# Performance work log

Hardware: AMD Instinct MI355X
Metric: run time of the kernel (lower is better)

The kernel has to match this reference:

```python
import jax, jax.numpy as jnp
import numpy as np

NEG = -9e15
ALPHA = 0.2  # leaky relu negative slope


def setup_inputs() -> dict:
    key = jax.random.key(0)
    k1, k2, k3, k4 = jax.random.split(key, 4)
    B, N, d = 8, 2048, 128
    h = jax.random.normal(k1, (B, N, d), dtype=jnp.float32)
    adj = jax.random.randint(k2, (B, N, N), 0, 2, dtype=jnp.int32)
    W = jax.random.normal(k3, (d, d), dtype=jnp.float32) * (1.414 / np.sqrt(d))
    a = jax.random.normal(k4, (2 * d, 1), dtype=jnp.float32) * 0.1
    return {"h": h, "adj": adj, "W": W, "a": a}


def reference(h, adj, W, a):
    d = W.shape[1]
    Wh = jnp.matmul(h, W)                       # [B, N, d]  (dropout p=0 -> identity)
    Wh1 = jnp.matmul(Wh, a[:d])                 # [B, N, 1]
    Wh2 = jnp.matmul(Wh, a[d:])                 # [B, N, 1]
    e = jax.nn.leaky_relu(Wh1 + jnp.swapaxes(Wh2, 1, 2), negative_slope=ALPHA)  # [B, N, N]
    scores = jnp.where(adj > 0, e, NEG)
    attention = jax.nn.softmax(scores, axis=-1)  # [B, N, N]
    h_prime = jnp.matmul(attention, Wh)          # [B, N, d]
    out = h + h_prime                            # residual=True, concat=False
    return out, attention
```

## Files before the change

### kernel.cpp

```cpp
#include <hip/hip_runtime.h>
#include <cstdint>
#include <cstddef>

typedef float  v4f __attribute__((ext_vector_type(4)));
typedef short  v8s __attribute__((ext_vector_type(8)));
typedef int    v4i __attribute__((ext_vector_type(4)));
typedef unsigned int v2u __attribute__((ext_vector_type(2)));

#define BB 8
#define NN 2048
#define DD 128
#define TI 16
#define NEGV (-9e15f)

__device__ __forceinline__ unsigned short f2bf(float x) {
  unsigned u = __float_as_uint(x);
  u = u + 0x7FFFu + ((u >> 16) & 1u);
  return (unsigned short)(u >> 16);
}

__global__ __launch_bounds__(256) void gat_k1(
    const float* __restrict__ h, const float* __restrict__ W, const float* __restrict__ a,
    short* __restrict__ whbT, float* __restrict__ wh1g, float* __restrict__ wh2g)
{
  __shared__ __align__(16) unsigned short wT[DD * 136];
  __shared__ __align__(16) unsigned short staging[DD * 72];

  const int tid  = threadIdx.x;
  const int lane = tid & 63;
  const int wid  = tid >> 6;
  const int m16  = lane & 15;
  const int quad = lane >> 4;
  const int b    = blockIdx.y;
  const int i0   = blockIdx.x * 64;

  {
    const v4f* W4 = (const v4f*)W;
    #pragma unroll
    for (int it = 0; it < 16; it++) {
      int idx = it * 256 + tid;
      int k  = idx >> 5;
      int c4 = (idx & 31) * 4;
      v4f wv = W4[idx];
      #pragma unroll
      for (int q = 0; q < 4; q++)
        wT[(c4 + q) * 136 + k] = f2bf(wv[q]);
    }
  }

  const float* hrow = h + (size_t)(b * NN + i0 + wid * 16 + m16) * DD;
  v8s af[4];
  #pragma unroll
  for (int ks = 0; ks < 4; ks++) {
    v4f x0 = *(const v4f*)(hrow + ks * 32 + quad * 8);
    v4f x1 = *(const v4f*)(hrow + ks * 32 + quad * 8 + 4);
    v8s t;
    t[0] = (short)f2bf(x0.x); t[1] = (short)f2bf(x0.y);
    t[2] = (short)f2bf(x0.z); t[3] = (short)f2bf(x0.w);
    t[4] = (short)f2bf(x1.x); t[5] = (short)f2bf(x1.y);
    t[6] = (short)f2bf(x1.z); t[7] = (short)f2bf(x1.w);
    af[ks] = t;
  }
  __syncthreads();

  v4f acc[8];
  #pragma unroll
  for (int t = 0; t < 8; t++) acc[t] = (v4f){0.f, 0.f, 0.f, 0.f};

  #pragma unroll
  for (int ks = 0; ks < 4; ks++) {
    #pragma unroll
    for (int t = 0; t < 8; t++) {
      v8s bf = *(const v8s*)&wT[(t * 16 + m16) * 136 + ks * 32 + quad * 8];
      acc[t] = __builtin_amdgcn_mfma_f32_16x16x32_bf16(af[ks], bf, acc[t], 0, 0, 0);
    }
  }

  {
    float a1v[8], a2v[8];
    #pragma unroll
    for (int t = 0; t < 8; t++) {
      a1v[t] = a[t * 16 + m16];
      a2v[t] = a[DD + t * 16 + m16];
    }
    #pragma unroll
    for (int r = 0; r < 4; r++) {
      float p1 = 0.f, p2 = 0.f;
      #pragma unroll
      for (int t = 0; t < 8; t++) {
        p1 += acc[t][r] * a1v[t];
        p2 += acc[t][r] * a2v[t];
      }
      #pragma unroll
      for (int off = 8; off > 0; off >>= 1) {
        p1 += __shfl_xor(p1, off);
        p2 += __shfl_xor(p2, off);
      }
      if (m16 == 0) {
        int gi = b * NN + i0 + wid * 16 + quad * 4 + r;
        wh1g[gi] = p1;
        wh2g[gi] = p2;
      }
    }
  }

  #pragma unroll
  for (int t = 0; t < 8; t++)
    #pragma unroll
    for (int r = 0; r < 4; r++)
      staging[(t * 16 + m16) * 72 + wid * 16 + quad * 4 + r] = f2bf(acc[t][r]);
  __syncthreads();

  #pragma unroll
  for (int it = 0; it < 4; it++) {
    int idx = it * 256 + tid;
    int c  = idx >> 3;
    int i8 = idx & 7;
    v8s val = *(const v8s*)&staging[c * 72 + i8 * 8];
    *(v8s*)(whbT + (size_t)b * DD * NN + (size_t)c * NN + i0 + i8 * 8) = val;
  }
}

__global__ __launch_bounds__(256) void gat_k2(
    const float* __restrict__ h, const int* __restrict__ adj,
    const short* __restrict__ whbT, const float* __restrict__ wh1g,
    const float* __restrict__ wh2g, float* __restrict__ out,
    float* __restrict__ attout)
{
  __shared__ __align__(16) float wh2s[NN];
  __shared__ float wh1s[TI];
  __shared__ unsigned int maskw[TI * 64];
  __shared__ float m_s[TI];
  __shared__ float rs_s[TI];
  __shared__ __align__(16) unsigned short atile[2][TI * 72];

  const int tid = threadIdx.x;
  const int lane = tid & 63;
  const int wid = tid >> 6;
  const int b = blockIdx.y;
  const int i0 = blockIdx.x * TI;

  {
    const v4f* w2g4 = (const v4f*)(wh2g + (size_t)b * NN);
    ((v4f*)wh2s)[tid] = w2g4[tid];
    ((v4f*)wh2s)[tid + 256] = w2g4[tid + 256];
  }
  if (tid < TI) wh1s[tid] = wh1g[b * NN + i0 + tid];
  __syncthreads();

  for (int ii = wid; ii < TI; ii += 4) {
    const v4i* arow = (const v4i*)(adj + (size_t)(b * NN + i0 + ii) * NN);
    const float wh1v = wh1s[ii];
    float e[32];
    float m = -INFINITY;
    unsigned mbits = 0u;
    #pragma unroll
    for (int u = 0; u < 8; u++) {
      v4i av = __builtin_nontemporal_load(&arow[u * 64 + lane]);
      v4f w2v = ((const v4f*)wh2s)[u * 64 + lane];
      #pragma unroll
      for (int q = 0; q < 4; q++) {
        bool mk = av[q] > 0;
        float x = wh1v + w2v[q];
        float ev = mk ? (x > 0.f ? x : 0.2f * x) : NEGV;
        e[u * 4 + q] = ev;
        m = fmaxf(m, ev);
        mbits |= (mk ? 1u : 0u) << (u * 4 + q);
      }
    }
    maskw[ii * 64 + lane] = mbits;
    #pragma unroll
    for (int off = 32; off > 0; off >>= 1) m = fmaxf(m, __shfl_xor(m, off));
    float s = 0.f;
    #pragma unroll
    for (int k = 0; k < 32; k++) s += __expf(e[k] - m);
    #pragma unroll
    for (int off = 32; off > 0; off >>= 1) s += __shfl_xor(s, off);
    if (lane == 0) { m_s[ii] = m; rs_s[ii] = 1.f / s; }
  }
  __syncthreads();

  float* attrow_base = attout + (size_t)(b * NN + i0) * NN;
  const short* whbT_b = whbT + (size_t)b * DD * NN;
  const int m16 = lane & 15;
  const int quad = lane >> 4;
  const int irow = tid >> 4;
  const int jq = tid & 15;
  const float wh1v = wh1s[irow];
  const float mi_r = m_s[irow];
  const float rsi_r = rs_s[irow];

  v4f acc[2];
  acc[0] = (v4f){0.f, 0.f, 0.f, 0.f};
  acc[1] = (v4f){0.f, 0.f, 0.f, 0.f};

  for (int jc = 0; jc < 32; jc++) {
    const int j0 = jc * 64;
    const int ubit = (jc >> 2) << 2;
    unsigned short* buf = atile[jc & 1];

    {
      unsigned mw = maskw[irow * 64 + ((jc * 16 + jq) & 63)];
      v4f w2v = ((const v4f*)wh2s)[(j0 >> 2) + jq];
      v4f av;
      unsigned short ab[4];
      #pragma unroll
      for (int q = 0; q < 4; q++) {
        float x = wh1v + w2v[q];
        float ev = ((mw >> (ubit + q)) & 1u) ? (x > 0.f ? x : 0.2f * x) : NEGV;
        float at = __expf(ev - mi_r) * rsi_r;
        av[q] = at;
        ab[q] = f2bf(at);
      }
      __builtin_nontemporal_store(av, (v4f*)(attrow_base + (size_t)irow * NN + j0 + jq * 4));
      v2u uv;
      uv[0] = (unsigned)ab[0] | ((unsigned)ab[1] << 16);
      uv[1] = (unsigned)ab[2] | ((unsigned)ab[3] << 16);
      *(v2u*)&buf[irow * 72 + jq * 4] = uv;
    }

    v8s bfr[2][2];
    #pragma unroll
    for (int ks = 0; ks < 2; ks++)
      #pragma unroll
      for (int t = 0; t < 2; t++)
        bfr[ks][t] = *(const v8s*)(whbT_b + (size_t)((wid * 2 + t) * 16 + m16) * NN
                                   + j0 + ks * 32 + quad * 8);

    __syncthreads();

    #pragma unroll
    for (int ks = 0; ks < 2; ks++) {
      v8s af = *(const v8s*)&buf[m16 * 72 + ks * 32 + quad * 8];
      acc[0] = __builtin_amdgcn_mfma_f32_16x16x32_bf16(af, bfr[ks][0], acc[0], 0, 0, 0);
      acc[1] = __builtin_amdgcn_mfma_f32_16x16x32_bf16(af, bfr[ks][1], acc[1], 0, 0, 0);
    }
  }

  #pragma unroll
  for (int t = 0; t < 2; t++) {
    #pragma unroll
    for (int r = 0; r < 4; r++) {
      size_t gidx = ((size_t)(b * NN + i0 + quad * 4 + r)) * DD + (wid * 2 + t) * 16 + m16;
      out[gidx] = h[gidx] + acc[t][r];
    }
  }
}

extern "C" void kernel_launch(void* const* d_in, const int* in_sizes, int n_in,
                              void* d_out, int out_size, void* d_ws, size_t ws_size,
                              hipStream_t stream) {
  const float* h  = (const float*)d_in[0];
  const int* adj  = (const int*)d_in[1];
  const float* W  = (const float*)d_in[2];
  const float* a  = (const float*)d_in[3];

  float* out    = (float*)d_out;
  float* attout = out + (size_t)BB * NN * DD;

  short* whbT = (short*)d_ws;
  float* wh1  = (float*)((char*)d_ws + (size_t)BB * DD * NN * 2);
  float* wh2  = wh1 + BB * NN;

  gat_k1<<<dim3(NN / 64, BB), 256, 0, stream>>>(h, W, a, whbT, wh1, wh2);
  gat_k2<<<dim3(NN / TI, BB), 256, 0, stream>>>(h, adj, whbT, wh1, wh2, out, attout);
}
```

Measured before the change: 285.2 us.

## Split softmax statistics into separate kernel and split-K the attention-value matmul across waves

Moves the adjacency scan, mask packing and row max/sum computation into a new kernel that writes bit masks and statistics to workspace. The main kernel then has each wave cover a quarter of the key dimension for all 128 output columns, building its MFMA A-operand in registers instead of a shared tile. This removes the per-chunk block barrier. Partial sums are reduced through shared memory before the residual add. It adds a kernel launch and workspace traffic, and raises register and LDS use.

```diff
diff --git a/kernel.cpp b/kernel.cpp
--- a/kernel.cpp
+++ b/kernel.cpp
@@ -5,7 +5,6 @@
 typedef float  v4f __attribute__((ext_vector_type(4)));
 typedef short  v8s __attribute__((ext_vector_type(8)));
 typedef int    v4i __attribute__((ext_vector_type(4)));
-typedef unsigned int v2u __attribute__((ext_vector_type(2)));
 
 #define BB 8
 #define NN 2048
@@ -121,128 +120,164 @@
   }
 }
 
-__global__ __launch_bounds__(256) void gat_k2(
-    const float* __restrict__ h, const int* __restrict__ adj,
+__global__ __launch_bounds__(256) void gat_k0(
+    const int* __restrict__ adj, const float* __restrict__ wh1g,
+    const float* __restrict__ wh2g, unsigned* __restrict__ maskg,
+    float* __restrict__ msg, float* __restrict__ rsg)
+{
+  const int tid  = threadIdx.x;
+  const int lane = tid & 63;
+  const int wid  = tid >> 6;
+  const int b    = blockIdx.y;
+  const int i    = blockIdx.x * 4 + wid;
+  const size_t row = (size_t)b * NN + i;
+
+  const v4i* arow = (const v4i*)(adj + row * NN);
+  const v4f* w2   = (const v4f*)(wh2g + (size_t)b * NN);
+  const float wh1v = wh1g[row];
+
+  float e[32];
+  float m = -INFINITY;
+  unsigned mbits = 0u;
+  #pragma unroll
+  for (int u = 0; u < 8; u++) {
+    v4i av  = __builtin_nontemporal_load(&arow[u * 64 + lane]);
+    v4f w2v = w2[u * 64 + lane];
+    #pragma unroll
+    for (int q = 0; q < 4; q++) {
+      bool mk = av[q] > 0;
+      float x = wh1v + w2v[q];
+      float ev = mk ? (x > 0.f ? x : 0.2f * x) : NEGV;
+      e[u * 4 + q] = ev;
+      m = fmaxf(m, ev);
+      mbits |= (mk ? 1u : 0u) << (u * 4 + q);
+    }
+  }
+  maskg[row * 64 + lane] = mbits;
+
+  #pragma unroll
+  for (int off = 32; off > 0; off >>= 1) m = fmaxf(m, __shfl_xor(m, off));
+  float s = 0.f;
+  #pragma unroll
+  for (int k = 0; k < 32; k++) s += __expf(e[k] - m);
+  #pragma unroll
+  for (int off = 32; off > 0; off >>= 1) s += __shfl_xor(s, off);
+
+  if (lane == 0) { msg[row] = m; rsg[row] = 1.f / s; }
+}
+
+__global__ __launch_bounds__(256, 4) void gat_k2(
+    const float* __restrict__ h, const unsigned* __restrict__ maskg,
     const short* __restrict__ whbT, const float* __restrict__ wh1g,
-    const float* __restrict__ wh2g, float* __restrict__ out,
+    const float* __restrict__ wh2g, const float* __restrict__ msg,
+    const float* __restrict__ rsg, float* __restrict__ out,
     float* __restrict__ attout)
 {
-  __shared__ __align__(16) float wh2s[NN];
-  __shared__ float wh1s[TI];
-  __shared__ unsigned int maskw[TI * 64];
-  __shared__ float m_s[TI];
-  __shared__ float rs_s[TI];
-  __shared__ __align__(16) unsigned short atile[2][TI * 72];
-
-  const int tid = threadIdx.x;
+  __shared__ __align__(16) float smem[4 * TI * DD];
+  __shared__ unsigned masks[TI * 68];
+  __shared__ float wh1s[TI], ms_s[TI], rs_s[TI];
+
+  const int tid  = threadIdx.x;
   const int lane = tid & 63;
-  const int wid = tid >> 6;
-  const int b = blockIdx.y;
-  const int i0 = blockIdx.x * TI;
-
+  const int wid  = tid >> 6;
+  const int m16  = lane & 15;
+  const int quad = lane >> 4;
+  const int b    = blockIdx.y;
+  const int i0   = blockIdx.x * TI;
+
+  float* wh2s = smem;
   {
     const v4f* w2g4 = (const v4f*)(wh2g + (size_t)b * NN);
-    ((v4f*)wh2s)[tid] = w2g4[tid];
+    ((v4f*)wh2s)[tid]       = w2g4[tid];
     ((v4f*)wh2s)[tid + 256] = w2g4[tid + 256];
   }
-  if (tid < TI) wh1s[tid] = wh1g[b * NN + i0 + tid];
-  __syncthreads();
-
-  for (int ii = wid; ii < TI; ii += 4) {
-    const v4i* arow = (const v4i*)(adj + (size_t)(b * NN + i0 + ii) * NN);
-    const float wh1v = wh1s[ii];
-    float e[32];
-    float m = -INFINITY;
-    unsigned mbits = 0u;
-    #pragma unroll
-    for (int u = 0; u < 8; u++) {
-      v4i av = __builtin_nontemporal_load(&arow[u * 64 + lane]);
-      v4f w2v = ((const v4f*)wh2s)[u * 64 + lane];
+  {
+    const unsigned* mg = maskg + (size_t)(b * NN + i0) * 64;
+    #pragma unroll
+    for (int it = 0; it < 4; it++) {
+      int idx = it * 256 + tid;
+      masks[(idx >> 6) * 68 + (idx & 63)] = mg[idx];
+    }
+  }
+  if (tid < TI) {
+    wh1s[tid] = wh1g[b * NN + i0 + tid];
+    ms_s[tid] = msg[b * NN + i0 + tid];
+    rs_s[tid] = rsg[b * NN + i0 + tid];
+  }
+  __syncthreads();
+
+  const float wh1v = wh1s[m16];
+  const float mi   = ms_s[m16];
+  const float rsi  = rs_s[m16];
+  const short* whbT_b = whbT + (size_t)b * DD * NN;
+  float* attrow = attout + (size_t)(b * NN + i0 + m16) * NN;
+
+  v4f acc[8];
+  #pragma unroll
+  for (int t = 0; t < 8; t++) acc[t] = (v4f){0.f, 0.f, 0.f, 0.f};
+
+  for (int c = 0; c < 8; c++) {
+    const int j0   = wid * 512 + c * 64;
+    const int ubit = (j0 >> 8) << 2;
+    #pragma unroll
+    for (int ks = 0; ks < 2; ks++) {
+      const int jb = j0 + ks * 32 + quad * 8;
+      v4f w2a = ((const v4f*)wh2s)[jb >> 2];
+      v4f w2b = ((const v4f*)wh2s)[(jb >> 2) + 1];
+      const int w0  = (jb >> 2) & 63;
+      unsigned mwa = masks[m16 * 68 + w0];
+      unsigned mwb = masks[m16 * 68 + w0 + 1];
+
+      v4f at0, at1;
+      v8s af;
       #pragma unroll
       for (int q = 0; q < 4; q++) {
-        bool mk = av[q] > 0;
-        float x = wh1v + w2v[q];
-        float ev = mk ? (x > 0.f ? x : 0.2f * x) : NEGV;
-        e[u * 4 + q] = ev;
-        m = fmaxf(m, ev);
-        mbits |= (mk ? 1u : 0u) << (u * 4 + q);
-      }
-    }
-    maskw[ii * 64 + lane] = mbits;
-    #pragma unroll
-    for (int off = 32; off > 0; off >>= 1) m = fmaxf(m, __shfl_xor(m, off));
-    float s = 0.f;
-    #pragma unroll
-    for (int k = 0; k < 32; k++) s += __expf(e[k] - m);
-    #pragma unroll
-    for (int off = 32; off > 0; off >>= 1) s += __shfl_xor(s, off);
-    if (lane == 0) { m_s[ii] = m; rs_s[ii] = 1.f / s; }
-  }
-  __syncthreads();
-
-  float* attrow_base = attout + (size_t)(b * NN + i0) * NN;
-  const short* whbT_b = whbT + (size_t)b * DD * NN;
-  const int m16 = lane & 15;
-  const int quad = lane >> 4;
-  const int irow = tid >> 4;
-  const int jq = tid & 15;
-  const float wh1v = wh1s[irow];
-  const float mi_r = m_s[irow];
-  const float rsi_r = rs_s[irow];
-
-  v4f acc[2];
-  acc[0] = (v4f){0.f, 0.f, 0.f, 0.f};
-  acc[1] = (v4f){0.f, 0.f, 0.f, 0.f};
-
-  for (int jc = 0; jc < 32; jc++) {
-    const int j0 = jc * 64;
-    const int ubit = (jc >> 2) << 2;
-    unsigned short* buf = atile[jc & 1];
-
-    {
-      unsigned mw = maskw[irow * 64 + ((jc * 16 + jq) & 63)];
-      v4f w2v = ((const v4f*)wh2s)[(j0 >> 2) + jq];
-      v4f av;
-      unsigned short ab[4];
+        float x = wh1v + w2a[q];
+        float ev = ((mwa >> (ubit + q)) & 1u) ? (x > 0.f ? x : 0.2f * x) : NEGV;
+        float at = __expf(ev - mi) * rsi;
+        at0[q] = at;
+        af[q]  = (short)f2bf(at);
+      }
       #pragma unroll
       for (int q = 0; q < 4; q++) {
-        float x = wh1v + w2v[q];
-        float ev = ((mw >> (ubit + q)) & 1u) ? (x > 0.f ? x : 0.2f * x) : NEGV;
-        float at = __expf(ev - mi_r) * rsi_r;
-        av[q] = at;
-        ab[q] = f2bf(at);
-      }
-      __builtin_nontemporal_store(av, (v4f*)(attrow_base + (size_t)irow * NN + j0 + jq * 4));
-      v2u uv;
-      uv[0] = (unsigned)ab[0] | ((unsigned)ab[1] << 16);
-      uv[1] = (unsigned)ab[2] | ((unsigned)ab[3] << 16);
-      *(v2u*)&buf[irow * 72 + jq * 4] = uv;
-    }
-
-    v8s bfr[2][2];
-    #pragma unroll
-    for (int ks = 0; ks < 2; ks++)
-      #pragma unroll
-      for (int t = 0; t < 2; t++)
-        bfr[ks][t] = *(const v8s*)(whbT_b + (size_t)((wid * 2 + t) * 16 + m16) * NN
-                                   + j0 + ks * 32 + quad * 8);
-
-    __syncthreads();
-
-    #pragma unroll
-    for (int ks = 0; ks < 2; ks++) {
-      v8s af = *(const v8s*)&buf[m16 * 72 + ks * 32 + quad * 8];
-      acc[0] = __builtin_amdgcn_mfma_f32_16x16x32_bf16(af, bfr[ks][0], acc[0], 0, 0, 0);
-      acc[1] = __builtin_amdgcn_mfma_f32_16x16x32_bf16(af, bfr[ks][1], acc[1], 0, 0, 0);
-    }
-  }
-
-  #pragma unroll
-  for (int t = 0; t < 2; t++) {
-    #pragma unroll
-    for (int r = 0; r < 4; r++) {
-      size_t gidx = ((size_t)(b * NN + i0 + quad * 4 + r)) * DD + (wid * 2 + t) * 16 + m16;
-      out[gidx] = h[gidx] + acc[t][r];
+        float x = wh1v + w2b[q];
+        float ev = ((mwb >> (ubit + q)) & 1u) ? (x > 0.f ? x : 0.2f * x) : NEGV;
+        float at = __expf(ev - mi) * rsi;
+        at1[q] = at;
+        af[4 + q] = (short)f2bf(at);
+      }
+      __builtin_nontemporal_store(at0, (v4f*)(attrow + jb));
+      __builtin_nontemporal_store(at1, (v4f*)(attrow + jb + 4));
+
+      #pragma unroll
+      for (int t = 0; t < 8; t++) {
+        v8s bf = *(const v8s*)(whbT_b + (size_t)(t * 16 + m16) * NN + jb);
+        acc[t] = __builtin_amdgcn_mfma_f32_16x16x32_bf16(af, bf, acc[t], 0, 0, 0);
+      }
+    }
+  }
+
+  __syncthreads();
+  float* red = smem;
+  #pragma unroll
+  for (int t = 0; t < 8; t++)
+    #pragma unroll
+    for (int r = 0; r < 4; r++)
+      red[wid * (TI * DD) + (quad * 4 + r) * DD + t * 16 + m16] = acc[t][r];
+  __syncthreads();
+
+  {
+    const size_t base = (size_t)(b * NN + i0) * DD;
+    #pragma unroll
+    for (int it = 0; it < 2; it++) {
+      int idx = it * 256 + tid;
+      v4f s0 = ((const v4f*)red)[idx];
+      v4f s1 = ((const v4f*)red)[idx + 512];
+      v4f s2 = ((const v4f*)red)[idx + 1024];
+      v4f s3 = ((const v4f*)red)[idx + 1536];
+      v4f hv = *(const v4f*)(h + base + (size_t)idx * 4);
+      v4f o  = hv + s0 + s1 + s2 + s3;
+      *(v4f*)(out + base + (size_t)idx * 4) = o;
     }
   }
 }
@@ -258,10 +293,15 @@
   float* out    = (float*)d_out;
   float* attout = out + (size_t)BB * NN * DD;
 
-  short* whbT = (short*)d_ws;
-  float* wh1  = (float*)((char*)d_ws + (size_t)BB * DD * NN * 2);
-  float* wh2  = wh1 + BB * NN;
+  char* ws = (char*)d_ws;
+  short* whbT = (short*)ws;                      ws += (size_t)BB * DD * NN * 2;
+  float* wh1  = (float*)ws;                      ws += (size_t)BB * NN * 4;
+  float* wh2  = (float*)ws;                      ws += (size_t)BB * NN * 4;
+  float* msg  = (float*)ws;                      ws += (size_t)BB * NN * 4;
+  float* rsg  = (float*)ws;                      ws += (size_t)BB * NN * 4;
+  unsigned* maskg = (unsigned*)ws;
 
   gat_k1<<<dim3(NN / 64, BB), 256, 0, stream>>>(h, W, a, whbT, wh1, wh2);
-  gat_k2<<<dim3(NN / TI, BB), 256, 0, stream>>>(h, adj, whbT, wh1, wh2, out, attout);
-}
+  gat_k0<<<dim3(NN / 4, BB), 256, 0, stream>>>(adj, wh1, wh2, maskg, msg, rsg);
+  gat_k2<<<dim3(NN / TI, BB), 256, 0, stream>>>(h, maskg, whbT, wh1, wh2, msg, rsg, out, attout);
+}
```

Measured after the change: 296.0 us. +3.8%, slower.
